# Kernel tuning notes

Hardware: AMD Instinct MI355X
Metric: run time of the kernel (lower is better)

The kernel has to match this reference:

```python
import jax, jax.numpy as jnp
import numpy as np

ALPHA = 1000.0  # softmin temperature from the original module


def setup_inputs() -> dict:
    key = jax.random.key(0)
    ks = jax.random.split(key, 10)
    B, D, H, E, K = 8192, 784, 256, 32, 512
    s = 0.05  # small init scale to keep activations/distances numerically sane
    return {
        "x": jax.random.normal(ks[0], (B, D), jnp.float32),
        "cluster_reps": jax.random.normal(ks[1], (K, E), jnp.float32),
        "W1": jax.random.normal(ks[2], (D, H), jnp.float32) * s,
        "b1": jnp.zeros((H,), jnp.float32),
        "W2": jax.random.normal(ks[3], (H, E), jnp.float32) * s,
        "b2": jnp.zeros((E,), jnp.float32),
        "W3": jax.random.normal(ks[4], (E, H), jnp.float32) * s,
        "b3": jnp.zeros((H,), jnp.float32),
        "W4": jax.random.normal(ks[5], (H, D), jnp.float32) * s,
        "b4": jnp.zeros((D,), jnp.float32),
    }


def reference(x, cluster_reps, W1, b1, W2, b2, W3, b3, W4, b4):
    # --- autoencoder: 2-layer MLP encoder / decoder ---
    h = jax.nn.relu(x @ W1 + b1)            # [B, H]
    embeddings = h @ W2 + b2                # [B, E]
    h2 = jax.nn.relu(embeddings @ W3 + b3)  # [B, H]
    reconstruction = h2 @ W4 + b4           # [B, D]

    # --- squared distances to cluster reps: [B, K] ---
    diff = embeddings[:, None, :] - cluster_reps[None, :, :]  # [B, K, E]
    distances = jnp.sum(diff * diff, axis=2)                  # [B, K]

    # --- stable softmin-weighted distances ---
    min_dist = jnp.min(distances, axis=1, keepdims=True)       # [B, 1]
    exponentials = jnp.exp(-ALPHA * (distances - min_dist))    # [B, K]
    sum_exponentials = jnp.sum(exponentials, axis=1, keepdims=True)
    weighted_dists = distances * (exponentials / sum_exponentials)

    return (weighted_dists, distances, reconstruction, embeddings)
```

## Files before the change

kernel.cpp:

```cpp
#include <hip/hip_runtime.h>
#include <cstddef>

#define NB 8192
#define ND 784
#define NH 256
#define NE 32
#define NK 512
#define ALPHA_F 1000.0f

typedef _Float16 h8 __attribute__((ext_vector_type(8)));
typedef float f32x4 __attribute__((ext_vector_type(4)));

#define TW1 25
#define TN1 8
#define NBW1 200
#define TW4 8
#define TN4 25
#define NBW4 200
#define NBW2 8
#define NBW3 8

__global__ __launch_bounds__(256)
void prep4_kernel(const float* __restrict__ W1, _Float16* __restrict__ w1thi,
                  _Float16* __restrict__ w1tlo,
                  const float* __restrict__ W4, _Float16* __restrict__ w4thi,
                  _Float16* __restrict__ w4tlo,
                  const float* __restrict__ W2, _Float16* __restrict__ w2thi,
                  _Float16* __restrict__ w2tlo,
                  const float* __restrict__ W3, _Float16* __restrict__ w3thi,
                  _Float16* __restrict__ w3tlo) {
    __shared__ float tile[32][33];
    const int b   = blockIdx.x;
    const int tid = threadIdx.x;

    const float* W; _Float16 *hi, *lo; int K, N, kt, nt;
    if (b < NBW1) {
        W = W1; hi = w1thi; lo = w1tlo; K = ND; N = NH;
        kt = b % TW1; nt = b / TW1;
    } else if (b < NBW1 + NBW4) {
        const int bb = b - NBW1;
        W = W4; hi = w4thi; lo = w4tlo; K = NH; N = ND;
        kt = bb % TW4; nt = bb / TW4;
    } else if (b < NBW1 + NBW4 + NBW2) {
        W = W2; hi = w2thi; lo = w2tlo; K = NH; N = NE;
        kt = b - (NBW1 + NBW4); nt = 0;
    } else {
        W = W3; hi = w3thi; lo = w3tlo; K = NE; N = NH;
        kt = 0; nt = b - (NBW1 + NBW4 + NBW2);
    }
    const int k0 = kt * 32, n0 = nt * 32;
    const int row = tid >> 3, c4 = (tid & 7) * 4;
    #pragma unroll
    for (int j = 0; j < 4; ++j) {
        const int k = k0 + row, n = n0 + c4 + j;
        tile[row][c4 + j] = (k < K && n < N) ? W[(size_t)k * N + n] : 0.f;
    }
    __syncthreads();
    const int n = n0 + row;
    if (n < N) {
        #pragma unroll
        for (int j = 0; j < 4; ++j) {
            const int k = k0 + c4 + j;
            if (k < K) {
                float w = tile[c4 + j][row];
                _Float16 hh = (_Float16)w;
                float r = w - (float)hh;
                hi[(size_t)n * K + k] = hh;
                lo[(size_t)n * K + k] = (_Float16)(r * 2048.0f);
            }
        }
    }
}

#define HSTR 264

__global__ __launch_bounds__(1024, 4)
void mega_kernel(const float* __restrict__ x, const float* __restrict__ reps,
                 const _Float16* __restrict__ w1thi, const _Float16* __restrict__ w1tlo,
                 const _Float16* __restrict__ w2thi, const _Float16* __restrict__ w2tlo,
                 const _Float16* __restrict__ w3thi, const _Float16* __restrict__ w3tlo,
                 const _Float16* __restrict__ w4thi, const _Float16* __restrict__ w4tlo,
                 const float* __restrict__ b1, const float* __restrict__ b2,
                 const float* __restrict__ b3, const float* __restrict__ b4,
                 float* __restrict__ emb_g, float* __restrict__ recon_g,
                 float* __restrict__ dist_g, float* __restrict__ wout_g) {
    __shared__ __align__(16) unsigned char lds[135936];
    _Float16* R0h  = (_Float16*)lds;
    _Float16* sA   = (_Float16*)(lds + 81920);
    _Float16* hP   = (_Float16*)(lds + 92160);
    float*    es   = (float*)(lds + 125952);
    _Float16* eh   = (_Float16*)(lds + 130560);
    _Float16* el   = (_Float16*)(lds + 133120);
    float*    rmin = (float*)(lds + 135680);
    float*    rinv = (float*)(lds + 135808);

    const int tid  = threadIdx.x;
    const int lane = tid & 63;
    const int wv   = tid >> 6;
    const int li   = lane & 15;
    const int kq   = (lane >> 4) * 8;
    const int quad = lane >> 4;
    const int r0   = blockIdx.x * 32;

    const float c1 = 1.0f / 2048.0f;
    const float c2 = c1 * c1;

    {
        _Float16* sBhi = R0h;
        _Float16* sBlo = R0h + 2 * 256 * 40;
        _Float16* sAhi = sA;
        _Float16* sAlo = sA + 2 * 32 * 40;
        const int arow = (tid & 255) >> 3;
        const int aro  = tid >> 2;
        const int ak   = (tid & 3) * 8;
        const int brow = tid >> 2;
        const int bk   = (tid & 3) * 8;
        (void)arow;
        const float*    pA  = x + (size_t)(r0 + aro) * ND;
        const _Float16* pBh = w1thi + (size_t)brow * ND;
        const _Float16* pBl = w1tlo + (size_t)brow * ND;

        float araw[8];
        h8 rbh, rbl;

        auto pf = [&](int s) {
            if (tid < 128) {
                const int k = s * 32 + ak;
                if (k + 8 <= ND) {
                    f32x4 v0 = *(const f32x4*)(pA + k);
                    f32x4 v1 = *(const f32x4*)(pA + k + 4);
                    #pragma unroll
                    for (int j = 0; j < 4; ++j) {
                        araw[j] = v0[j]; araw[4 + j] = v1[j];
                    }
                } else {
                    #pragma unroll
                    for (int j = 0; j < 8; ++j) araw[j] = 0.f;
                }
            }
            const int kb = s * 32 + bk;
            rbh = (kb + 8 <= ND) ? *(const h8*)(pBh + kb) : (h8){};
            rbl = (kb + 8 <= ND) ? *(const h8*)(pBl + kb) : (h8){};
        };
        auto cm = [&](int buf) {
            if (tid < 128) {
                h8 hi, lo;
                #pragma unroll
                for (int j = 0; j < 8; ++j) {
                    float v = araw[j];
                    _Float16 hh = (_Float16)v;
                    hi[j] = hh;
                    lo[j] = (_Float16)((v - (float)hh) * 2048.0f);
                }
                *(h8*)&sAhi[buf * 32 * 40 + aro * 40 + ak] = hi;
                *(h8*)&sAlo[buf * 32 * 40 + aro * 40 + ak] = lo;
            }
            *(h8*)&sBhi[buf * 256 * 40 + brow * 40 + bk] = rbh;
            *(h8*)&sBlo[buf * 256 * 40 + brow * 40 + bk] = rbl;
        };

        pf(0); cm(0); pf(1);
        __syncthreads();

        f32x4 a0[2] = {}, a1[2] = {}, a2[2] = {};
        for (int s = 0; s < 25; ++s) {
            const int buf = s & 1;
            h8 fah[2], fal[2];
            #pragma unroll
            for (int mt = 0; mt < 2; ++mt) {
                const int ao = buf * 32 * 40 + (mt * 16 + li) * 40 + kq;
                fah[mt] = *(const h8*)&sAhi[ao];
                fal[mt] = *(const h8*)&sAlo[ao];
            }
            const int bo = buf * 256 * 40 + (wv * 16 + li) * 40 + kq;
            h8 fbh = *(const h8*)&sBhi[bo];
            h8 fbl = *(const h8*)&sBlo[bo];
            #pragma unroll
            for (int mt = 0; mt < 2; ++mt) {
                a0[mt] = __builtin_amdgcn_mfma_f32_16x16x32_f16(fah[mt], fbh, a0[mt], 0, 0, 0);
                a1[mt] = __builtin_amdgcn_mfma_f32_16x16x32_f16(fah[mt], fbl, a1[mt], 0, 0, 0);
                a1[mt] = __builtin_amdgcn_mfma_f32_16x16x32_f16(fal[mt], fbh, a1[mt], 0, 0, 0);
                a2[mt] = __builtin_amdgcn_mfma_f32_16x16x32_f16(fal[mt], fbl, a2[mt], 0, 0, 0);
            }
            if (s + 1 < 25) { cm((s + 1) & 1); if (s + 2 < 25) pf(s + 2); }
            __syncthreads();
        }
        _Float16* hhi = hP;
        _Float16* hlo = hP + 32 * HSTR;
        const int n = wv * 16 + li;
        const float bv = b1[n];
        #pragma unroll
        for (int mt = 0; mt < 2; ++mt)
            #pragma unroll
            for (int r = 0; r < 4; ++r) {
                const int m = mt * 16 + quad * 4 + r;
                float v = a0[mt][r] + c1 * a1[mt][r] + c2 * a2[mt][r] + bv;
                v = fmaxf(v, 0.f);
                _Float16 t = (_Float16)v;
                hhi[m * HSTR + n] = t;
                hlo[m * HSTR + n] = (_Float16)((v - (float)t) * 2048.0f);
            }
    }
    __syncthreads();

    {
        _Float16* w2h = R0h;
        _Float16* w2l = R0h + 32 * HSTR;
        const int row = tid >> 5, off = (tid & 31) * 8;
        *(h8*)&w2h[row * HSTR + off] = *(const h8*)(w2thi + row * 256 + off);
        *(h8*)&w2l[row * HSTR + off] = *(const h8*)(w2tlo + row * 256 + off);
    }
    __syncthreads();
    if (wv < 4) {
        const int mt = wv >> 1, nt = wv & 1;
        _Float16* hhi = hP;
        _Float16* hlo = hP + 32 * HSTR;
        _Float16* w2h = R0h;
        _Float16* w2l = R0h + 32 * HSTR;
        f32x4 e0 = {}, e1 = {}, e2 = {};
        #pragma unroll
        for (int ks = 0; ks < 8; ++ks) {
            const int k = ks * 32 + kq;
            h8 ah = *(const h8*)&hhi[(mt * 16 + li) * HSTR + k];
            h8 al = *(const h8*)&hlo[(mt * 16 + li) * HSTR + k];
            h8 bh = *(const h8*)&w2h[(nt * 16 + li) * HSTR + k];
            h8 bl = *(const h8*)&w2l[(nt * 16 + li) * HSTR + k];
            e0 = __builtin_amdgcn_mfma_f32_16x16x32_f16(ah, bh, e0, 0, 0, 0);
            e1 = __builtin_amdgcn_mfma_f32_16x16x32_f16(ah, bl, e1, 0, 0, 0);
            e1 = __builtin_amdgcn_mfma_f32_16x16x32_f16(al, bh, e1, 0, 0, 0);
            e2 = __builtin_amdgcn_mfma_f32_16x16x32_f16(al, bl, e2, 0, 0, 0);
        }
        const int col = nt * 16 + li;
        const float bv = b2[col];
        #pragma unroll
        for (int r = 0; r < 4; ++r) {
            const int m = mt * 16 + quad * 4 + r;
            float v = e0[r] + c1 * e1[r] + c2 * e2[r] + bv;
            es[m * 36 + col] = v;
            _Float16 t = (_Float16)v;
            eh[m * 40 + col] = t;
            el[m * 40 + col] = (_Float16)((v - (float)t) * 2048.0f);
            emb_g[(size_t)(r0 + m) * NE + col] = v;
        }
    }
    __syncthreads();

    {
        _Float16* w3h = R0h;
        _Float16* w3l = R0h + 256 * 40;
        const int row = tid >> 2, off = (tid & 3) * 8;
        *(h8*)&w3h[row * 40 + off] = *(const h8*)(w3thi + row * 32 + off);
        *(h8*)&w3l[row * 40 + off] = *(const h8*)(w3tlo + row * 32 + off);
    }
    __syncthreads();
    {
        _Float16* w3h  = R0h;
        _Float16* w3l  = R0h + 256 * 40;
        _Float16* h2h  = hP;
        _Float16* h2l  = hP + 32 * HSTR;
        h8 ah[2], al[2];
        #pragma unroll
        for (int mt = 0; mt < 2; ++mt) {
            ah[mt] = *(const h8*)&eh[(mt * 16 + li) * 40 + kq];
            al[mt] = *(const h8*)&el[(mt * 16 + li) * 40 + kq];
        }
        const int col = wv * 16 + li;
        h8 bh = *(const h8*)&w3h[col * 40 + kq];
        h8 bl = *(const h8*)&w3l[col * 40 + kq];
        const float bv = b3[col];
        #pragma unroll
        for (int mt = 0; mt < 2; ++mt) {
            f32x4 q0 = {}, q1 = {}, q2 = {};
            q0 = __builtin_amdgcn_mfma_f32_16x16x32_f16(ah[mt], bh, q0, 0, 0, 0);
            q1 = __builtin_amdgcn_mfma_f32_16x16x32_f16(ah[mt], bl, q1, 0, 0, 0);
            q1 = __builtin_amdgcn_mfma_f32_16x16x32_f16(al[mt], bh, q1, 0, 0, 0);
            q2 = __builtin_amdgcn_mfma_f32_16x16x32_f16(al[mt], bl, q2, 0, 0, 0);
            #pragma unroll
            for (int r = 0; r < 4; ++r) {
                const int m = mt * 16 + quad * 4 + r;
                float v = q0[r] + c1 * q1[r] + c2 * q2[r] + bv;
                v = fmaxf(v, 0.f);
                _Float16 t = (_Float16)v;
                h2h[m * HSTR + col] = t;
                h2l[m * HSTR + col] = (_Float16)((v - (float)t) * 2048.0f);
            }
        }
    }
    __syncthreads();

    {
        _Float16* sBhi = R0h;
        _Float16* sBlo = R0h + 2 * 128 * 40;
        _Float16* h2h  = hP;
        _Float16* h2l  = hP + 32 * HSTR;
        const int mt  = wv >> 3;
        const int ntw = wv & 7;
        const int brow = tid >> 2;
        const int bk4  = (tid & 3) * 8;
        h8 rbh, rbl;
        auto pf = [&](int ss) {
            if (tid < 512) {
                int rg = (ss >> 3) * 128 + brow;
                if (rg > ND - 1) rg = ND - 1;
                const int k = (ss & 7) * 32 + bk4;
                rbh = *(const h8*)(w4thi + (size_t)rg * NH + k);
                rbl = *(const h8*)(w4tlo + (size_t)rg * NH + k);
            }
        };
        auto cm = [&](int ss) {
            if (tid < 512) {
                const int buf = ss & 1;
                *(h8*)&sBhi[buf * 128 * 40 + brow * 40 + bk4] = rbh;
                *(h8*)&sBlo[buf * 128 * 40 + brow * 40 + bk4] = rbl;
            }
        };
        pf(0); cm(0); pf(1);
        __syncthreads();

        f32x4 q0 = {}, q1 = {};
        for (int ss = 0; ss < 56; ++ss) {
            const int buf = ss & 1, ks = ss & 7;
            const int bo = buf * 128 * 40 + (ntw * 16 + li) * 40 + kq;
            h8 fbh = *(const h8*)&sBhi[bo];
            h8 fbl = *(const h8*)&sBlo[bo];
            const int k = ks * 32 + kq;
            h8 ah = *(const h8*)&h2h[(mt * 16 + li) * HSTR + k];
            h8 al = *(const h8*)&h2l[(mt * 16 + li) * HSTR + k];
            q0 = __builtin_amdgcn_mfma_f32_16x16x32_f16(ah, fbh, q0, 0, 0, 0);
            q1 = __builtin_amdgcn_mfma_f32_16x16x32_f16(ah, fbl, q1, 0, 0, 0);
            q1 = __builtin_amdgcn_mfma_f32_16x16x32_f16(al, fbh, q1, 0, 0, 0);
            if (ss + 1 < 56) { cm(ss + 1); if (ss + 2 < 56) pf(ss + 2); }
            __syncthreads();
            if (ks == 7) {
                const int n = (ss >> 3) * 128 + ntw * 16 + li;
                if (n < ND) {
                    const float bv = b4[n];
                    #pragma unroll
                    for (int r = 0; r < 4; ++r) {
                        const int m = mt * 16 + quad * 4 + r;
                        recon_g[(size_t)(r0 + m) * ND + n] = q0[r] + c1 * q1[r] + bv;
                    }
                }
                q0 = {}; q1 = {};
            }
        }
    }
    __syncthreads();

    {
        float* tr0 = (float*)lds;
        float* tr1 = (float*)(lds + 33280);
        const int half = tid >> 9;
        const int cl   = tid & 511;
        float* trh = half ? tr1 : tr0;
        const int rbase = half * 16;

        const float* rp = reps + (size_t)cl * NE;
        f32x4 rv[8];
        #pragma unroll
        for (int e4 = 0; e4 < 8; ++e4) rv[e4] = ((const f32x4*)rp)[e4];

        float d[16];
        #pragma unroll
        for (int r = 0; r < 16; ++r) {
            float a = 0.f;
            #pragma unroll
            for (int e4 = 0; e4 < 8; ++e4) {
                f32x4 ev = *(const f32x4*)&es[(rbase + r) * 36 + e4 * 4];
                #pragma unroll
                for (int j = 0; j < 4; ++j) {
                    float t = ev[j] - rv[e4][j];
                    a = fmaf(t, t, a);
                }
            }
            d[r] = a;
            trh[r * 520 + cl] = a;
        }
        __syncthreads();
        {
            const int w8 = wv & 7;
            #pragma unroll
            for (int p = 0; p < 2; ++p) {
                const int rl = w8 * 2 + p;
                float m = trh[rl * 520 + lane];
                #pragma unroll
                for (int j = 1; j < 8; ++j)
                    m = fminf(m, trh[rl * 520 + lane + 64 * j]);
                #pragma unroll
                for (int off = 32; off > 0; off >>= 1)
                    m = fminf(m, __shfl_xor(m, off, 64));
                if (lane == 0) rmin[rbase + rl] = m;
            }
        }
        __syncthreads();
        #pragma unroll
        for (int r = 0; r < 16; ++r)
            trh[r * 520 + cl] = expf(-ALPHA_F * (d[r] - rmin[rbase + r]));
        __syncthreads();
        {
            const int w8 = wv & 7;
            #pragma unroll
            for (int p = 0; p < 2; ++p) {
                const int rl = w8 * 2 + p;
                float s = trh[rl * 520 + lane];
                #pragma unroll
                for (int j = 1; j < 8; ++j)
                    s += trh[rl * 520 + lane + 64 * j];
                #pragma unroll
                for (int off = 32; off > 0; off >>= 1)
                    s += __shfl_xor(s, off, 64);
                if (lane == 0) rinv[rbase + rl] = 1.0f / s;
            }
        }
        __syncthreads();
        #pragma unroll
        for (int r = 0; r < 16; ++r) {
            const size_t row = (size_t)(r0 + rbase + r);
            const float ev = expf(-ALPHA_F * (d[r] - rmin[rbase + r]));
            dist_g[row * NK + cl] = d[r];
            wout_g[row * NK + cl] = d[r] * (ev * rinv[rbase + r]);
        }
    }
}

__global__ __launch_bounds__(256)
void splitw2_kernel(const float* __restrict__ W1, _Float16* __restrict__ w1thi,
                    _Float16* __restrict__ w1tlo,
                    const float* __restrict__ W4, _Float16* __restrict__ w4thi,
                    _Float16* __restrict__ w4tlo) {
    const int b = blockIdx.x;
    const float* W; _Float16 *hi, *lo; int K, N, n;
    if (b < NH) { W = W1; hi = w1thi; lo = w1tlo; K = ND; N = NH; n = b; }
    else        { W = W4; hi = w4thi; lo = w4tlo; K = NH; N = ND; n = b - NH; }
    for (int k = threadIdx.x; k < K; k += 256) {
        float w = W[(size_t)k * N + n];
        _Float16 hh = (_Float16)w;
        float r = w - (float)hh;
        hi[(size_t)n * K + k] = hh;
        lo[(size_t)n * K + k] = (_Float16)(r * 2048.0f);
    }
}

template<int TERMS, bool RELU, bool SPLITA, int MT>
__global__ __launch_bounds__(256)
void mfma_gemm3(const float* __restrict__ Af32,
                const _Float16* __restrict__ Ahi_g,
                const _Float16* __restrict__ Alo_g,
                const _Float16* __restrict__ WThi,
                const _Float16* __restrict__ WTlo,
                const float* __restrict__ bias, float* __restrict__ C,
                int N, int K, int KS) {
    constexpr int BM  = MT * 32;
    constexpr int ACH = BM / 64;
    constexpr int AS  = BM * 40;
    constexpr int BS  = 64 * 40;
    __shared__ __align__(16) _Float16 smem[2 * BM * 40 * 2 + 2 * 64 * 40 * 2];
    _Float16* sAhi = smem;
    _Float16* sAlo = sAhi + 2 * BM * 40;
    _Float16* sBhi = sAlo + 2 * BM * 40;
    _Float16* sBlo = sBhi + 2 * 64 * 40;

    const int tid = threadIdx.x;
    const int bm  = blockIdx.x * BM;
    const int bn  = blockIdx.y * 64;

    const int arow = (ACH == 1) ? (tid >> 2) : (tid >> 1);
    const int ak   = (ACH == 1) ? ((tid & 3) * 8) : ((tid & 1) * 16);
    const int brow = tid >> 2;
    const int bk   = (tid & 3) * 8;

    const float*    pA32 = SPLITA ? Af32 + (size_t)(bm + arow) * K : nullptr;
    const _Float16* pAhi = SPLITA ? nullptr : Ahi_g + (size_t)(bm + arow) * K;
    const _Float16* pAlo = SPLITA ? nullptr : Alo_g + (size_t)(bm + arow) * K;
    int brow_g = bn + brow; if (brow_g > N - 1) brow_g = N - 1;
    const _Float16* pBhi = WThi + (size_t)brow_g * K;
    const _Float16* pBlo = WTlo + (size_t)brow_g * K;

    float araw[ACH * 8];
    h8 rahi[ACH], ralo[ACH];
    h8 rbhi, rblo;

    auto prefetch = [&](int s) {
        #pragma unroll
        for (int c = 0; c < ACH; ++c) {
            const int k = s * 32 + ak + c * 8;
            if (SPLITA) {
                if (k + 8 <= K) {
                    f32x4 v0 = *(const f32x4*)(pA32 + k);
                    f32x4 v1 = *(const f32x4*)(pA32 + k + 4);
                    #pragma unroll
                    for (int j = 0; j < 4; ++j) {
                        araw[c * 8 + j]     = v0[j];
                        araw[c * 8 + 4 + j] = v1[j];
                    }
                } else {
                    #pragma unroll
                    for (int j = 0; j < 8; ++j) araw[c * 8 + j] = 0.f;
                }
            } else {
                rahi[c] = (k + 8 <= K) ? *(const h8*)(pAhi + k) : (h8){};
                ralo[c] = (k + 8 <= K) ? *(const h8*)(pAlo + k) : (h8){};
            }
        }
        const int kb = s * 32 + bk;
        rbhi = (kb + 8 <= K) ? *(const h8*)(pBhi + kb) : (h8){};
        rblo = (kb + 8 <= K) ? *(const h8*)(pBlo + kb) : (h8){};
    };

    auto commit = [&](int buf) {
        #pragma unroll
        for (int c = 0; c < ACH; ++c) {
            h8 hi, lo;
            if (SPLITA) {
                #pragma unroll
                for (int j = 0; j < 8; ++j) {
                    float v = araw[c * 8 + j];
                    _Float16 hh = (_Float16)v;
                    hi[j] = hh;
                    lo[j] = (_Float16)((v - (float)hh) * 2048.0f);
                }
            } else { hi = rahi[c]; lo = ralo[c]; }
            *(h8*)&sAhi[buf * AS + arow * 40 + ak + c * 8] = hi;
            *(h8*)&sAlo[buf * AS + arow * 40 + ak + c * 8] = lo;
        }
        *(h8*)&sBhi[buf * BS + brow * 40 + bk] = rbhi;
        *(h8*)&sBlo[buf * BS + brow * 40 + bk] = rblo;
    };

    prefetch(0);
    commit(0);
    prefetch(1);
    __syncthreads();

    const int lane = tid & 63;
    const int wv   = tid >> 6;
    const int wm   = (wv >> 1) * (MT * 16);
    const int wn   = (wv & 1) * 32;
    const int li   = lane & 15;
    const int kq   = (lane >> 4) * 8;

    f32x4 acc0[MT][2] = {};
    f32x4 acc1[MT][2] = {};
    f32x4 acc2[MT][2] = {};

    for (int s = 0; s < KS; ++s) {
        const int buf = s & 1;
        h8 fahi[MT], falo[MT], fbhi[2], fblo[2];
        #pragma unroll
        for (int mt = 0; mt < MT; ++mt) {
            const int ao = buf * AS + (wm + mt * 16 + li) * 40 + kq;
            fahi[mt] = *(const h8*)&sAhi[ao];
            falo[mt] = *(const h8*)&sAlo[ao];
        }
        #pragma unroll
        for (int nt = 0; nt < 2; ++nt) {
            const int bo = buf * BS + (wn + nt * 16 + li) * 40 + kq;
            fbhi[nt] = *(const h8*)&sBhi[bo];
            fblo[nt] = *(const h8*)&sBlo[bo];
        }
        #pragma unroll
        for (int mt = 0; mt < MT; ++mt)
            #pragma unroll
            for (int nt = 0; nt < 2; ++nt) {
                acc0[mt][nt] = __builtin_amdgcn_mfma_f32_16x16x32_f16(
                    fahi[mt], fbhi[nt], acc0[mt][nt], 0, 0, 0);
                acc1[mt][nt] = __builtin_amdgcn_mfma_f32_16x16x32_f16(
                    fahi[mt], fblo[nt], acc1[mt][nt], 0, 0, 0);
                acc1[mt][nt] = __builtin_amdgcn_mfma_f32_16x16x32_f16(
                    falo[mt], fbhi[nt], acc1[mt][nt], 0, 0, 0);
                if (TERMS == 4)
                    acc2[mt][nt] = __builtin_amdgcn_mfma_f32_16x16x32_f16(
                        falo[mt], fblo[nt], acc2[mt][nt], 0, 0, 0);
            }
        if (s + 1 < KS) {
            commit((s + 1) & 1);
            if (s + 2 < KS) prefetch(s + 2);
        }
        __syncthreads();
    }

    const float c1 = 1.0f / 2048.0f;
    const float c2 = c1 * c1;
    const int quad = lane >> 4;
    #pragma unroll
    for (int nt = 0; nt < 2; ++nt) {
        const int n = bn + wn + nt * 16 + li;
        if (n < N) {
            const float bv = bias[n];
            #pragma unroll
            for (int mt = 0; mt < MT; ++mt) {
                #pragma unroll
                for (int r = 0; r < 4; ++r) {
                    const int m = bm + wm + mt * 16 + quad * 4 + r;
                    float v = acc0[mt][nt][r] + c1 * acc1[mt][nt][r];
                    if (TERMS == 4) v += c2 * acc2[mt][nt][r];
                    v += bv;
                    if (RELU) v = fmaxf(v, 0.f);
                    C[(size_t)m * N + n] = v;
                }
            }
        }
    }
}

__global__ __launch_bounds__(256)
void mid_kernel(const float* __restrict__ h, const float* __restrict__ W2,
                const float* __restrict__ b2, const float* __restrict__ W3,
                const float* __restrict__ b3, float* __restrict__ emb,
                _Float16* __restrict__ h2hi, _Float16* __restrict__ h2lo) {
    __shared__ float es[16][32];
    const int tid = threadIdx.x;
    const int r0  = blockIdx.x * 16;

    #pragma unroll
    for (int half = 0; half < 2; ++half) {
        const int o   = tid + half * 256;
        const int row = o >> 5;
        const int col = o & 31;
        const float* hrow = h + (size_t)(r0 + row) * NH;
        float acc0 = 0.f, acc1 = 0.f;
        #pragma unroll 4
        for (int k = 0; k < NH; k += 4) {
            float4 hv = *(const float4*)(hrow + k);
            acc0 = fmaf(hv.x, W2[(k + 0) * NE + col], acc0);
            acc1 = fmaf(hv.y, W2[(k + 1) * NE + col], acc1);
            acc0 = fmaf(hv.z, W2[(k + 2) * NE + col], acc0);
            acc1 = fmaf(hv.w, W2[(k + 3) * NE + col], acc1);
        }
        float v = acc0 + acc1 + b2[col];
        es[row][col] = v;
        emb[(size_t)r0 * NE + o] = v;
    }
    __syncthreads();

    const int col = tid;
    float acc[16];
    #pragma unroll
    for (int r = 0; r < 16; ++r) acc[r] = 0.f;
    #pragma unroll
    for (int k = 0; k < NE; ++k) {
        float w = W3[k * NH + col];
        #pragma unroll
        for (int r = 0; r < 16; ++r) acc[r] = fmaf(es[r][k], w, acc[r]);
    }
    const float bb = b3[col];
    #pragma unroll
    for (int r = 0; r < 16; ++r) {
        float v = acc[r] + bb;
        v = v > 0.f ? v : 0.f;
        _Float16 hh = (_Float16)v;
        float rr = v - (float)hh;
        h2hi[(size_t)(r0 + r) * NH + col] = hh;
        h2lo[(size_t)(r0 + r) * NH + col] = (_Float16)(rr * 2048.0f);
    }
}

__global__ __launch_bounds__(512, 4)
void dist_kernel(const float* __restrict__ emb, const float* __restrict__ reps,
                 float* __restrict__ dist, float* __restrict__ wout) {
    __shared__ float es[8][32];
    __shared__ float tr[8][520];
    __shared__ float rmin[8];
    __shared__ float rinv[8];

    const int tid = threadIdx.x;
    const int r0  = blockIdx.x * 8;

    if (tid < 256) es[tid >> 5][tid & 31] = emb[(size_t)r0 * NE + tid];

    const float* rp = reps + (size_t)tid * NE;
    f32x4 rv[8];
    #pragma unroll
    for (int e4 = 0; e4 < 8; ++e4) rv[e4] = ((const f32x4*)rp)[e4];
    __syncthreads();

    float d[8];
    #pragma unroll
    for (int r = 0; r < 8; ++r) {
        float a = 0.f;
        #pragma unroll
        for (int e4 = 0; e4 < 8; ++e4) {
            f32x4 ev = *(const f32x4*)&es[r][e4 * 4];
            #pragma unroll
            for (int j = 0; j < 4; ++j) {
                float t = ev[j] - rv[e4][j];
                a = fmaf(t, t, a);
            }
        }
        d[r] = a;
    }

    const int lane = tid & 63;
    const int wv   = tid >> 6;

    #pragma unroll
    for (int r = 0; r < 8; ++r) tr[r][tid] = d[r];
    __syncthreads();
    {
        f32x4 a = *(const f32x4*)&tr[wv][lane * 8];
        f32x4 b = *(const f32x4*)&tr[wv][lane * 8 + 4];
        float m = fminf(fminf(fminf(a[0], a[1]), fminf(a[2], a[3])),
                        fminf(fminf(b[0], b[1]), fminf(b[2], b[3])));
        #pragma unroll
        for (int off = 32; off > 0; off >>= 1)
            m = fminf(m, __shfl_xor(m, off, 64));
        if (lane == 0) rmin[wv] = m;
    }
    __syncthreads();

    float e[8];
    #pragma unroll
    for (int r = 0; r < 8; ++r) {
        e[r] = expf(-ALPHA_F * (d[r] - rmin[r]));
        tr[r][tid] = e[r];
    }
    __syncthreads();
    {
        f32x4 a = *(const f32x4*)&tr[wv][lane * 8];
        f32x4 b = *(const f32x4*)&tr[wv][lane * 8 + 4];
        float s = ((a[0] + a[1]) + (a[2] + a[3])) +
                  ((b[0] + b[1]) + (b[2] + b[3]));
        #pragma unroll
        for (int off = 32; off > 0; off >>= 1)
            s += __shfl_xor(s, off, 64);
        if (lane == 0) rinv[wv] = 1.0f / s;
    }
    __syncthreads();

    #pragma unroll
    for (int r = 0; r < 8; ++r) {
        const size_t row = (size_t)(r0 + r);
        dist[row * NK + tid] = d[r];
        wout[row * NK + tid] = d[r] * (e[r] * rinv[r]);
    }
}

extern "C" void kernel_launch(void* const* d_in, const int* in_sizes, int n_in,
                              void* d_out, int out_size, void* d_ws, size_t ws_size,
                              hipStream_t stream) {
    const float* x    = (const float*)d_in[0];
    const float* reps = (const float*)d_in[1];
    const float* W1   = (const float*)d_in[2];
    const float* b1   = (const float*)d_in[3];
    const float* W2   = (const float*)d_in[4];
    const float* b2   = (const float*)d_in[5];
    const float* W3   = (const float*)d_in[6];
    const float* b3   = (const float*)d_in[7];
    const float* W4   = (const float*)d_in[8];
    const float* b4   = (const float*)d_in[9];

    float* out   = (float*)d_out;
    float* wout  = out;
    float* dist  = out + (size_t)NB * NK;
    float* recon = out + (size_t)2 * NB * NK;
    float* emb   = out + (size_t)2 * NB * NK + (size_t)NB * ND;

    const size_t nW14 = (size_t)ND * NH;
    const size_t nW23 = (size_t)NE * NH;
    const size_t wneed = (4 * nW14 + 4 * nW23) * sizeof(_Float16);

    if (d_ws != nullptr && ws_size >= wneed) {
        _Float16* w1thi = (_Float16*)d_ws;
        _Float16* w1tlo = w1thi + nW14;
        _Float16* w4thi = w1tlo + nW14;
        _Float16* w4tlo = w4thi + nW14;
        _Float16* w2thi = w4tlo + nW14;
        _Float16* w2tlo = w2thi + nW23;
        _Float16* w3thi = w2tlo + nW23;
        _Float16* w3tlo = w3thi + nW23;

        prep4_kernel<<<NBW1 + NBW4 + NBW2 + NBW3, 256, 0, stream>>>(
            W1, w1thi, w1tlo, W4, w4thi, w4tlo,
            W2, w2thi, w2tlo, W3, w3thi, w3tlo);

        mega_kernel<<<NB / 32, 1024, 0, stream>>>(
            x, reps, w1thi, w1tlo, w2thi, w2tlo, w3thi, w3tlo, w4thi, w4tlo,
            b1, b2, b3, b4, emb, recon, dist, wout);
    } else {
        float* h = dist;
        _Float16* h2hi  = (_Float16*)(dist + (size_t)NB * NH);
        _Float16* h2lo  = h2hi + (size_t)NB * NH;
        _Float16* w1thi = (_Float16*)wout;
        _Float16* w1tlo = w1thi + (size_t)NH * ND;
        _Float16* w4thi = w1tlo + (size_t)NH * ND;
        _Float16* w4tlo = w4thi + (size_t)ND * NH;

        splitw2_kernel<<<NH + ND, 256, 0, stream>>>(W1, w1thi, w1tlo,
                                                    W4, w4thi, w4tlo);
        mfma_gemm3<4, true, true, 2><<<dim3(128, 4), 256, 0, stream>>>(
            x, nullptr, nullptr, w1thi, w1tlo, b1, h, NH, ND, 25);
        mid_kernel<<<NB / 16, 256, 0, stream>>>(h, W2, b2, W3, b3,
                                                emb, h2hi, h2lo);
        mfma_gemm3<3, false, false, 4><<<dim3(64, 13), 256, 0, stream>>>(
            nullptr, h2hi, h2lo, w4thi, w4tlo, b4, recon, ND, NH, 8);
        dist_kernel<<<NB / 8, 512, 0, stream>>>(emb, reps, dist, wout);
    }
}
```

Before: 160.9 us.

## Deepen W4 decoder LDS pipeline to four slots, halve barriers, reuse stored exponentials

The decoder GEMM stage now uses a four-slot LDS ring with two register staging buffers. It runs two MFMA steps per barrier instead of one, which halves the number of __syncthreads in the 56-step loop and gives global prefetches more time to land. This doubles the LDS footprint for the W4 tiles. Separately, the softmin output reads exponentials already stored in the LDS transpose buffer instead of recomputing expf, which assumes that buffer holds the exp values and was not overwritten.

```diff
diff --git a/kernel.cpp b/kernel.cpp
--- a/kernel.cpp
+++ b/kernel.cpp
@@ -110,12 +110,10 @@
         _Float16* sBlo = R0h + 2 * 256 * 40;
         _Float16* sAhi = sA;
         _Float16* sAlo = sA + 2 * 32 * 40;
-        const int arow = (tid & 255) >> 3;
         const int aro  = tid >> 2;
         const int ak   = (tid & 3) * 8;
         const int brow = tid >> 2;
         const int bk   = (tid & 3) * 8;
-        (void)arow;
         const float*    pA  = x + (size_t)(r0 + aro) * ND;
         const _Float16* pBh = w1thi + (size_t)brow * ND;
         const _Float16* pBl = w1tlo + (size_t)brow * ND;
@@ -290,37 +288,37 @@
 
     {
         _Float16* sBhi = R0h;
-        _Float16* sBlo = R0h + 2 * 128 * 40;
+        _Float16* sBlo = R0h + 4 * 128 * 40;
         _Float16* h2h  = hP;
         _Float16* h2l  = hP + 32 * HSTR;
         const int mt  = wv >> 3;
         const int ntw = wv & 7;
         const int brow = tid >> 2;
         const int bk4  = (tid & 3) * 8;
-        h8 rbh, rbl;
+        h8 rbh[2], rbl[2];
         auto pf = [&](int ss) {
-            if (tid < 512) {
+            if (tid < 512 && ss < 56) {
                 int rg = (ss >> 3) * 128 + brow;
                 if (rg > ND - 1) rg = ND - 1;
                 const int k = (ss & 7) * 32 + bk4;
-                rbh = *(const h8*)(w4thi + (size_t)rg * NH + k);
-                rbl = *(const h8*)(w4tlo + (size_t)rg * NH + k);
+                rbh[ss & 1] = *(const h8*)(w4thi + (size_t)rg * NH + k);
+                rbl[ss & 1] = *(const h8*)(w4tlo + (size_t)rg * NH + k);
             }
         };
         auto cm = [&](int ss) {
-            if (tid < 512) {
-                const int buf = ss & 1;
-                *(h8*)&sBhi[buf * 128 * 40 + brow * 40 + bk4] = rbh;
-                *(h8*)&sBlo[buf * 128 * 40 + brow * 40 + bk4] = rbl;
+            if (tid < 512 && ss < 56) {
+                const int sl = ss & 3;
+                *(h8*)&sBhi[sl * 128 * 40 + brow * 40 + bk4] = rbh[ss & 1];
+                *(h8*)&sBlo[sl * 128 * 40 + brow * 40 + bk4] = rbl[ss & 1];
             }
         };
-        pf(0); cm(0); pf(1);
+        pf(0); pf(1); cm(0); cm(1); pf(2); pf(3);
         __syncthreads();
 
         f32x4 q0 = {}, q1 = {};
-        for (int ss = 0; ss < 56; ++ss) {
-            const int buf = ss & 1, ks = ss & 7;
-            const int bo = buf * 128 * 40 + (ntw * 16 + li) * 40 + kq;
+        auto step = [&](int t) {
+            const int sl = t & 3, ks = t & 7;
+            const int bo = sl * 128 * 40 + (ntw * 16 + li) * 40 + kq;
             h8 fbh = *(const h8*)&sBhi[bo];
             h8 fbl = *(const h8*)&sBlo[bo];
             const int k = ks * 32 + kq;
@@ -329,10 +327,8 @@
             q0 = __builtin_amdgcn_mfma_f32_16x16x32_f16(ah, fbh, q0, 0, 0, 0);
             q1 = __builtin_amdgcn_mfma_f32_16x16x32_f16(ah, fbl, q1, 0, 0, 0);
             q1 = __builtin_amdgcn_mfma_f32_16x16x32_f16(al, fbh, q1, 0, 0, 0);
-            if (ss + 1 < 56) { cm(ss + 1); if (ss + 2 < 56) pf(ss + 2); }
-            __syncthreads();
             if (ks == 7) {
-                const int n = (ss >> 3) * 128 + ntw * 16 + li;
+                const int n = (t >> 3) * 128 + ntw * 16 + li;
                 if (n < ND) {
                     const float bv = b4[n];
                     #pragma unroll
@@ -343,6 +339,14 @@
                 }
                 q0 = {}; q1 = {};
             }
+        };
+        for (int ii = 0; ii < 28; ++ii) {
+            const int s0 = ii * 2;
+            step(s0);
+            step(s0 + 1);
+            cm(s0 + 2); cm(s0 + 3);
+            pf(s0 + 4); pf(s0 + 5);
+            __syncthreads();
         }
     }
     __syncthreads();
@@ -416,7 +420,7 @@
         #pragma unroll
         for (int r = 0; r < 16; ++r) {
             const size_t row = (size_t)(r0 + rbase + r);
-            const float ev = expf(-ALPHA_F * (d[r] - rmin[rbase + r]));
+            const float ev = trh[r * 520 + cl];
             dist_g[row * NK + cl] = d[r];
             wout_g[row * NK + cl] = d[r] * (ev * rinv[rbase + r]);
         }
```

After: 162.5 us. Within noise of the previous version (+1.0%).
